# Kernel optimization log

Hardware: AMD Instinct MI355X
Metric: run time of the kernel (lower is better)

Reference implementation:

```python
import jax, jax.numpy as jnp
import numpy as np


def setup_inputs() -> dict:
    key = jax.random.key(0)
    k1, k2 = jax.random.split(key)
    B, T, F = 8, 1000, 257
    m = jax.random.normal(k1, (B, 27, T, F), dtype=jnp.float32)
    x = jax.random.normal(k2, (B, F, T, 2), dtype=jnp.float32)
    v = jnp.array([[1.0, -0.5, -0.5], [0.0, np.sqrt(3) / 2, -np.sqrt(3) / 2]], dtype=jnp.float32)
    return {"m": m, "x": x, "v": v}


def reference(m, x, v):
    B, C, T, F = m.shape
    # m -> (B, 3, 9, T, F); contract the complex-basis dim (3) with v rows
    m5 = m.reshape(B, 3, C // 3, T, F)
    H_real = jnp.einsum('k,bkntf->bntf', v[0], m5)  # (B, 9, T, F)
    H_imag = jnp.einsum('k,bkntf->bntf', v[1], m5)
    M_real = H_real.reshape(B, 3, 3, T, F)
    M_imag = H_imag.reshape(B, 3, 3, T, F)

    # x: (B,F,T,2) -> (B,2,T,F), pad: time causal (top=2), freq symmetric (1,1)
    xp = jnp.transpose(x, (0, 3, 2, 1))
    xp = jnp.pad(xp, ((0, 0), (0, 0), (2, 0), (1, 1)))
    # 3x3 unfold as 9 shifted views: (B, 2, 3, 3, T, F)
    xu = jnp.stack(
        [xp[:, :, i:i + T, j:j + F] for i in range(3) for j in range(3)],
        axis=2,
    ).reshape(B, 2, 3, 3, T, F)

    xr, xi = xu[:, 0], xu[:, 1]
    x_enh_real = jnp.sum(M_real * xr - M_imag * xi, axis=(1, 2))  # (B, T, F)
    x_enh_imag = jnp.sum(M_real * xi + M_imag * xr, axis=(1, 2))
    x_enh = jnp.stack([x_enh_real, x_enh_imag], axis=3)  # (B, T, F, 2)
    return jnp.transpose(x_enh, (0, 2, 1, 3))  # (B, F, T, 2)
```

## Files before the change

kernel.cpp:

```cpp
#include <hip/hip_runtime.h>


constexpr int B = 8, C = 27, T = 1000, F = 257;
constexpr int TCH = 8;
constexpr int NT  = T / TCH;
constexpr int BLK = 320;
constexpr int TROW  = 10;
constexpr int ROWSU = 259;
constexpr int RP    = 11;
constexpr int PLANE = 260 * RP;

__global__ __launch_bounds__(BLK, 4)
void ccm_kernel(const float* __restrict__ m,
                const float* __restrict__ x,
                float* __restrict__ out) {
    __shared__ float xs[2 * PLANE];

    const int bid = blockIdx.x;
    const int tc  = bid % NT;
    const int b   = bid / NT;
    const int t0  = tc * TCH;
    const int tx  = threadIdx.x;

    const float* xb = x + (size_t)b * F * T * 2;

    for (int p = tx; p < ROWSU * TROW; p += BLK) {
        const int row = p / TROW;
        const int tt  = p - row * TROW;
        const int f   = row - 1;
        const int t   = t0 - 2 + tt;
        float re = 0.f, im = 0.f;
        if (f >= 0 && f < F && t >= 0) {
            const float2 v = *reinterpret_cast<const float2*>(
                xb + ((size_t)f * T + t) * 2);
            re = v.x; im = v.y;
        }
        xs[row * RP + tt]         = re;
        xs[PLANE + row * RP + tt] = im;
    }
    __syncthreads();

    if (tx >= F) return;
    const int f = tx;

    const float SQ3_2 = 0.8660254037844386f;

    float wr[3][3], wi[3][3];
    #pragma unroll
    for (int p = 0; p < 2; ++p) {
        #pragma unroll
        for (int j = 0; j < 3; ++j) {
            wr[p][j] = xs[(f + j) * RP + p];
            wi[p][j] = xs[PLANE + (f + j) * RP + p];
        }
    }

    const float* mb = m + ((size_t)b * C * T + t0) * F + f;
    constexpr size_t CS = (size_t)T * F;

    float2 res[TCH];

    #pragma unroll
    for (int u = 0; u < TCH; ++u) {
        #pragma unroll
        for (int j = 0; j < 3; ++j) {
            wr[2][j] = xs[(f + j) * RP + (u + 2)];
            wi[2][j] = xs[PLANE + (f + j) * RP + (u + 2)];
        }

        float a0v[9], a1v[9], a2v[9];
        #pragma unroll
        for (int n = 0; n < 9; ++n) {
            a0v[n] = mb[(size_t)(0 * 9 + n) * CS + (size_t)u * F];
            a1v[n] = mb[(size_t)(1 * 9 + n) * CS + (size_t)u * F];
            a2v[n] = mb[(size_t)(2 * 9 + n) * CS + (size_t)u * F];
        }

        float accr = 0.f, acci = 0.f;
        #pragma unroll
        for (int i = 0; i < 3; ++i) {
            #pragma unroll
            for (int j = 0; j < 3; ++j) {
                const int n = i * 3 + j;
                const float hr = a0v[n] - 0.5f * (a1v[n] + a2v[n]);
                const float hi = SQ3_2 * (a1v[n] - a2v[n]);
                accr += hr * wr[i][j] - hi * wi[i][j];
                acci += hr * wi[i][j] + hi * wr[i][j];
            }
        }
        res[u] = make_float2(accr, acci);

        #pragma unroll
        for (int j = 0; j < 3; ++j) {
            wr[0][j] = wr[1][j]; wi[0][j] = wi[1][j];
            wr[1][j] = wr[2][j]; wi[1][j] = wi[2][j];
        }
    }

    float* op = out + ((size_t)(b * F + f) * T + t0) * 2;
    #pragma unroll
    for (int u = 0; u < TCH / 2; ++u) {
        reinterpret_cast<float4*>(op)[u] =
            make_float4(res[2 * u].x, res[2 * u].y,
                        res[2 * u + 1].x, res[2 * u + 1].y);
    }
}

extern "C" void kernel_launch(void* const* d_in, const int* in_sizes, int n_in,
                              void* d_out, int out_size, void* d_ws, size_t ws_size,
                              hipStream_t stream) {
    const float* m = (const float*)d_in[0];
    const float* x = (const float*)d_in[1];
    float* out = (float*)d_out;

    const int grid = B * NT;
    ccm_kernel<<<grid, BLK, 0, stream>>>(m, x, out);
}
```

Baseline: 68.05 us.

## Halve time chunk and double-buffer m loads across time steps

Reduces the per-block time chunk from 8 to 4, doubling the grid size, and shrinks the shared tile padding to match. The m loads are restructured into explicit double-buffered register arrays so the next step's 27 loads are issued before the current step's compute. The aim is more blocks in flight and more memory-level parallelism in this bandwidth-bound kernel. In exchange, x halo rows are reloaded more often relative to useful work, and more registers are held live.

```diff
diff --git a/kernel.cpp b/kernel.cpp
--- a/kernel.cpp
+++ b/kernel.cpp
@@ -2,12 +2,12 @@
 
 
 constexpr int B = 8, C = 27, T = 1000, F = 257;
-constexpr int TCH = 8;
+constexpr int TCH = 4;
 constexpr int NT  = T / TCH;
 constexpr int BLK = 320;
-constexpr int TROW  = 10;
+constexpr int TROW  = TCH + 2;
 constexpr int ROWSU = 259;
-constexpr int RP    = 11;
+constexpr int RP    = 7;
 constexpr int PLANE = 260 * RP;
 
 __global__ __launch_bounds__(BLK, 4)
@@ -44,6 +44,8 @@
     const int f = tx;
 
     const float SQ3_2 = 0.8660254037844386f;
+    constexpr size_t CS = (size_t)T * F;
+    const float* mb = m + ((size_t)b * C * T + t0) * F;
 
     float wr[3][3], wi[3][3];
     #pragma unroll
@@ -55,47 +57,51 @@
         }
     }
 
-    const float* mb = m + ((size_t)b * C * T + t0) * F + f;
-    constexpr size_t CS = (size_t)T * F;
-
     float2 res[TCH];
 
-    #pragma unroll
-    for (int u = 0; u < TCH; ++u) {
-        #pragma unroll
-        for (int j = 0; j < 3; ++j) {
-            wr[2][j] = xs[(f + j) * RP + (u + 2)];
-            wi[2][j] = xs[PLANE + (f + j) * RP + (u + 2)];
-        }
+#define LOADM(DST, U)                                                     \
+    {                                                                     \
+        _Pragma("unroll")                                                 \
+        for (int n = 0; n < 27; ++n)                                      \
+            DST[n] = mb[(size_t)n * CS + (size_t)(U) * F + f];            \
+    }
 
-        float a0v[9], a1v[9], a2v[9];
-        #pragma unroll
-        for (int n = 0; n < 9; ++n) {
-            a0v[n] = mb[(size_t)(0 * 9 + n) * CS + (size_t)u * F];
-            a1v[n] = mb[(size_t)(1 * 9 + n) * CS + (size_t)u * F];
-            a2v[n] = mb[(size_t)(2 * 9 + n) * CS + (size_t)u * F];
-        }
+#define STEP(AV, U)                                                       \
+    {                                                                     \
+        _Pragma("unroll")                                                 \
+        for (int j = 0; j < 3; ++j) {                                     \
+            wr[2][j] = xs[(f + j) * RP + ((U) + 2)];                      \
+            wi[2][j] = xs[PLANE + (f + j) * RP + ((U) + 2)];              \
+        }                                                                 \
+        float accr = 0.f, acci = 0.f;                                     \
+        _Pragma("unroll")                                                 \
+        for (int i = 0; i < 3; ++i) {                                     \
+            _Pragma("unroll")                                             \
+            for (int j = 0; j < 3; ++j) {                                 \
+                const int n = i * 3 + j;                                  \
+                const float hr = AV[n] - 0.5f * (AV[n + 9] + AV[n + 18]); \
+                const float hi = SQ3_2 * (AV[n + 9] - AV[n + 18]);        \
+                accr += hr * wr[i][j] - hi * wi[i][j];                    \
+                acci += hr * wi[i][j] + hi * wr[i][j];                    \
+            }                                                             \
+        }                                                                 \
+        res[U] = make_float2(accr, acci);                                 \
+        _Pragma("unroll")                                                 \
+        for (int j = 0; j < 3; ++j) {                                     \
+            wr[0][j] = wr[1][j]; wi[0][j] = wi[1][j];                     \
+            wr[1][j] = wr[2][j]; wi[1][j] = wi[2][j];                     \
+        }                                                                 \
+    }
 
-        float accr = 0.f, acci = 0.f;
-        #pragma unroll
-        for (int i = 0; i < 3; ++i) {
-            #pragma unroll
-            for (int j = 0; j < 3; ++j) {
-                const int n = i * 3 + j;
-                const float hr = a0v[n] - 0.5f * (a1v[n] + a2v[n]);
-                const float hi = SQ3_2 * (a1v[n] - a2v[n]);
-                accr += hr * wr[i][j] - hi * wi[i][j];
-                acci += hr * wi[i][j] + hi * wr[i][j];
-            }
-        }
-        res[u] = make_float2(accr, acci);
+    float Am[27], Bm[27];
+    LOADM(Am, 0);
+    LOADM(Bm, 1);  STEP(Am, 0);
+    LOADM(Am, 2);  STEP(Bm, 1);
+    LOADM(Bm, 3);  STEP(Am, 2);
+                   STEP(Bm, 3);
 
-        #pragma unroll
-        for (int j = 0; j < 3; ++j) {
-            wr[0][j] = wr[1][j]; wi[0][j] = wi[1][j];
-            wr[1][j] = wr[2][j]; wi[1][j] = wi[2][j];
-        }
-    }
+#undef LOADM
+#undef STEP
 
     float* op = out + ((size_t)(b * F + f) * T + t0) * 2;
     #pragma unroll
```

Result: faster. 59.26 us (-12.9%).

## Vectorize m loads by flattening time-frequency chunk into float4 per thread

Applied to the files above, without the earlier changes.

Each thread now owns four consecutive elements of the flattened (time, freq) chunk, so m is read with 128-bit loads instead of scalar ones. The time chunk per block drops from 8 to 4, the x tile is staged with float4 loads into an XOR-swizzled shared layout, and m loads are interleaved with the multiply-accumulate work. The aim is fewer, wider memory transactions on the dominant m stream and more blocks in flight. In exchange there is a slow path for threads whose four elements wrap across a row boundary, and output stores become strided float2 writes.

```diff
diff --git a/kernel.cpp b/kernel.cpp
--- a/kernel.cpp
+++ b/kernel.cpp
@@ -2,19 +2,25 @@
 
 
 constexpr int B = 8, C = 27, T = 1000, F = 257;
-constexpr int TCH = 8;
+constexpr int TCH = 4;
 constexpr int NT  = T / TCH;
 constexpr int BLK = 320;
-constexpr int TROW  = 10;
-constexpr int ROWSU = 259;
-constexpr int RP    = 11;
-constexpr int PLANE = 260 * RP;
+constexpr int NA  = 257;
+constexpr int TROW = TCH + 2;
+constexpr int FP   = 260;
+constexpr int PLSZ = TROW * FP + 32;
+constexpr size_t CS = (size_t)T * F;
 
-__global__ __launch_bounds__(BLK, 4)
+__device__ __forceinline__ int XSW(int a) { return a ^ (((a >> 5) & 7) << 2); }
+__device__ __forceinline__ float comp(const float4& v, int r) {
+    return r == 0 ? v.x : (r == 1 ? v.y : (r == 2 ? v.z : v.w));
+}
+
+__global__ __launch_bounds__(BLK, 3)
 void ccm_kernel(const float* __restrict__ m,
                 const float* __restrict__ x,
                 float* __restrict__ out) {
-    __shared__ float xs[2 * PLANE];
+    __shared__ float xs[2 * PLSZ];
 
     const int bid = blockIdx.x;
     const int tc  = bid % NT;
@@ -24,85 +30,134 @@
 
     const float* xb = x + (size_t)b * F * T * 2;
 
-    for (int p = tx; p < ROWSU * TROW; p += BLK) {
-        const int row = p / TROW;
-        const int tt  = p - row * TROW;
-        const int f   = row - 1;
-        const int t   = t0 - 2 + tt;
-        float re = 0.f, im = 0.f;
-        if (f >= 0 && f < F && t >= 0) {
-            const float2 v = *reinterpret_cast<const float2*>(
-                xb + ((size_t)f * T + t) * 2);
-            re = v.x; im = v.y;
+    if (tx < 259) {
+        const int f = tx - 1;
+        float vre[6], vim[6];
+        #pragma unroll
+        for (int tt = 0; tt < 6; ++tt) { vre[tt] = 0.f; vim[tt] = 0.f; }
+        if (f >= 0 && f < F) {
+            if (t0 >= 2) {
+                const float4* src = reinterpret_cast<const float4*>(
+                    xb + ((size_t)f * T + (t0 - 2)) * 2);
+                const float4 p0 = src[0], p1 = src[1], p2 = src[2];
+                vre[0] = p0.x; vim[0] = p0.y; vre[1] = p0.z; vim[1] = p0.w;
+                vre[2] = p1.x; vim[2] = p1.y; vre[3] = p1.z; vim[3] = p1.w;
+                vre[4] = p2.x; vim[4] = p2.y; vre[5] = p2.z; vim[5] = p2.w;
+            } else {
+                #pragma unroll
+                for (int tt = 0; tt < 6; ++tt) {
+                    const int t = t0 - 2 + tt;
+                    if (t >= 0) {
+                        const float2 v2 = *reinterpret_cast<const float2*>(
+                            xb + ((size_t)f * T + t) * 2);
+                        vre[tt] = v2.x; vim[tt] = v2.y;
+                    }
+                }
+            }
         }
-        xs[row * RP + tt]         = re;
-        xs[PLANE + row * RP + tt] = im;
+        #pragma unroll
+        for (int tt = 0; tt < 6; ++tt) {
+            const int a = XSW(tt * FP + tx);
+            xs[a]        = vre[tt];
+            xs[PLSZ + a] = vim[tt];
+        }
     }
     __syncthreads();
 
-    if (tx >= F) return;
-    const int f = tx;
+    if (tx >= NA) return;
+
+    const int e0 = 4 * tx;
+    const int tl = e0 / 257;
+    const int f0 = e0 - tl * 257;
 
     const float SQ3_2 = 0.8660254037844386f;
+    const float* mseg = m + (size_t)b * C * CS + (size_t)t0 * F + 4 * tx;
 
-    float wr[3][3], wi[3][3];
-    #pragma unroll
-    for (int p = 0; p < 2; ++p) {
-        #pragma unroll
-        for (int j = 0; j < 3; ++j) {
-            wr[p][j] = xs[(f + j) * RP + p];
-            wi[p][j] = xs[PLANE + (f + j) * RP + p];
-        }
+    float4 g[9][3];
+#define LOADG(n)                                                            \
+    {                                                                       \
+        g[n][0] = *reinterpret_cast<const float4*>(mseg + (size_t)(n) * CS);       \
+        g[n][1] = *reinterpret_cast<const float4*>(mseg + (size_t)((n) + 9) * CS); \
+        g[n][2] = *reinterpret_cast<const float4*>(mseg + (size_t)((n) + 18) * CS);\
     }
 
-    const float* mb = m + ((size_t)b * C * T + t0) * F + f;
-    constexpr size_t CS = (size_t)T * F;
+#define MAC_N(n, WRE, WIE)                                                  \
+    {                                                                       \
+        constexpr int i_ = (n) / 3, j_ = (n) % 3;                           \
+        _Pragma("unroll")                                                   \
+        for (int r = 0; r < 4; ++r) {                                       \
+            const float a0 = comp(g[n][0], r);                              \
+            const float a1 = comp(g[n][1], r);                              \
+            const float a2 = comp(g[n][2], r);                              \
+            const float hr = a0 - 0.5f * (a1 + a2);                         \
+            const float hi = SQ3_2 * (a1 - a2);                             \
+            accr[r] += hr * WRE(r, i_, j_) - hi * WIE(r, i_, j_);           \
+            acci[r] += hr * WIE(r, i_, j_) + hi * WRE(r, i_, j_);           \
+        }                                                                   \
+    }
 
-    float2 res[TCH];
+    float accr[4] = {0.f, 0.f, 0.f, 0.f};
+    float acci[4] = {0.f, 0.f, 0.f, 0.f};
+
+    LOADG(0); LOADG(1); LOADG(2);
+
+    if (f0 <= 253) {
+        float wr[3][6], wi[3][6];
+        #pragma unroll
+        for (int i = 0; i < 3; ++i) {
+            const int rowb = (tl + i) * FP + f0;
+            #pragma unroll
+            for (int k = 0; k < 6; ++k) {
+                const int a = XSW(rowb + k);
+                wr[i][k] = xs[a];
+                wi[i][k] = xs[PLSZ + a];
+            }
+        }
+#define WF_R(r, i, j) wr[i][(r) + (j)]
+#define WF_I(r, i, j) wi[i][(r) + (j)]
+        LOADG(3); MAC_N(0, WF_R, WF_I);
+        LOADG(4); MAC_N(1, WF_R, WF_I);
+        LOADG(5); MAC_N(2, WF_R, WF_I);
+        LOADG(6); MAC_N(3, WF_R, WF_I);
+        LOADG(7); MAC_N(4, WF_R, WF_I);
+        LOADG(8); MAC_N(5, WF_R, WF_I);
+        MAC_N(6, WF_R, WF_I);
+        MAC_N(7, WF_R, WF_I);
+        MAC_N(8, WF_R, WF_I);
+#undef WF_R
+#undef WF_I
+    } else {
+        int tlr_[4], fr_[4];
+        #pragma unroll
+        for (int r = 0; r < 4; ++r) {
+            const int w = (f0 + r) >= 257 ? 1 : 0;
+            tlr_[r] = tl + w;
+            fr_[r]  = f0 + r - 257 * w;
+        }
+#define WS_R(r, i, j) xs[XSW((tlr_[r] + (i)) * FP + fr_[r] + (j))]
+#define WS_I(r, i, j) xs[PLSZ + XSW((tlr_[r] + (i)) * FP + fr_[r] + (j))]
+        LOADG(3); MAC_N(0, WS_R, WS_I);
+        LOADG(4); MAC_N(1, WS_R, WS_I);
+        LOADG(5); MAC_N(2, WS_R, WS_I);
+        LOADG(6); MAC_N(3, WS_R, WS_I);
+        LOADG(7); MAC_N(4, WS_R, WS_I);
+        LOADG(8); MAC_N(5, WS_R, WS_I);
+        MAC_N(6, WS_R, WS_I);
+        MAC_N(7, WS_R, WS_I);
+        MAC_N(8, WS_R, WS_I);
+#undef WS_R
+#undef WS_I
+    }
+#undef LOADG
+#undef MAC_N
 
     #pragma unroll
-    for (int u = 0; u < TCH; ++u) {
-        #pragma unroll
-        for (int j = 0; j < 3; ++j) {
-            wr[2][j] = xs[(f + j) * RP + (u + 2)];
-            wi[2][j] = xs[PLANE + (f + j) * RP + (u + 2)];
-        }
-
-        float a0v[9], a1v[9], a2v[9];
-        #pragma unroll
-        for (int n = 0; n < 9; ++n) {
-            a0v[n] = mb[(size_t)(0 * 9 + n) * CS + (size_t)u * F];
-            a1v[n] = mb[(size_t)(1 * 9 + n) * CS + (size_t)u * F];
-            a2v[n] = mb[(size_t)(2 * 9 + n) * CS + (size_t)u * F];
-        }
-
-        float accr = 0.f, acci = 0.f;
-        #pragma unroll
-        for (int i = 0; i < 3; ++i) {
-            #pragma unroll
-            for (int j = 0; j < 3; ++j) {
-                const int n = i * 3 + j;
-                const float hr = a0v[n] - 0.5f * (a1v[n] + a2v[n]);
-                const float hi = SQ3_2 * (a1v[n] - a2v[n]);
-                accr += hr * wr[i][j] - hi * wi[i][j];
-                acci += hr * wi[i][j] + hi * wr[i][j];
-            }
-        }
-        res[u] = make_float2(accr, acci);
-
-        #pragma unroll
-        for (int j = 0; j < 3; ++j) {
-            wr[0][j] = wr[1][j]; wi[0][j] = wi[1][j];
-            wr[1][j] = wr[2][j]; wi[1][j] = wi[2][j];
-        }
-    }
-
-    float* op = out + ((size_t)(b * F + f) * T + t0) * 2;
-    #pragma unroll
-    for (int u = 0; u < TCH / 2; ++u) {
-        reinterpret_cast<float4*>(op)[u] =
-            make_float4(res[2 * u].x, res[2 * u].y,
-                        res[2 * u + 1].x, res[2 * u + 1].y);
+    for (int r = 0; r < 4; ++r) {
+        const int w  = (f0 + r) >= 257 ? 1 : 0;
+        const int fr = f0 + r - 257 * w;
+        const int tr = t0 + tl + w;
+        *reinterpret_cast<float2*>(out + ((size_t)(b * F + fr) * T + tr) * 2) =
+            make_float2(accr[r], acci[r]);
     }
 }
 
```

After: 66.66 us. 2.0% less time.
